# Optimization experiments

Hardware: AMD Instinct MI355X
Metric: run time of the kernel (lower is better)

Reference implementation:

```python
import jax, jax.numpy as jnp
import numpy as np

MODES = 256
WIDTH = 64
T_HIST = 1
T_FUT = 1
BATCH = 64
S = 8192


def setup_inputs() -> dict:
    key = jax.random.key(0)
    ks = jax.random.split(key, 12)
    scale = 1.0 / (WIDTH * WIDTH)
    inp = {
        "u": jax.random.normal(ks[0], (BATCH, S, T_HIST), dtype=jnp.float32),
        # lifting layer: Linear(T_HIST+1 -> WIDTH), stored [in, out]
        "fc0_w": jax.random.normal(ks[1], (T_HIST + 1, WIDTH), dtype=jnp.float32) * 0.5,
        "fc0_b": jax.random.normal(ks[2], (WIDTH,), dtype=jnp.float32) * 0.1,
        # 4 spectral conv layers, complex weights stored as real/imag parts
        "sw_r": scale * jax.random.uniform(ks[3], (4, WIDTH, WIDTH, MODES), dtype=jnp.float32),
        "sw_i": scale * jax.random.uniform(ks[4], (4, WIDTH, WIDTH, MODES), dtype=jnp.float32),
        # 4 pointwise (1x1 conv) layers: weight [out,in], bias [out]
        "pw_w": jax.random.normal(ks[5], (4, WIDTH, WIDTH), dtype=jnp.float32) * (1.0 / np.sqrt(WIDTH)),
        "pw_b": jax.random.normal(ks[6], (4, WIDTH), dtype=jnp.float32) * 0.1,
        # projection head
        "fc1_w": jax.random.normal(ks[7], (WIDTH, 128), dtype=jnp.float32) * (1.0 / np.sqrt(WIDTH)),
        "fc1_b": jax.random.normal(ks[8], (128,), dtype=jnp.float32) * 0.1,
        "fc2_w": jax.random.normal(ks[9], (128, T_FUT), dtype=jnp.float32) * (1.0 / np.sqrt(128)),
        "fc2_b": jax.random.normal(ks[10], (T_FUT,), dtype=jnp.float32) * 0.1,
    }
    return inp


def _spectral_conv(x, wr, wi):
    # x: [b, c_in, s] real; weights: [c_in, c_out, MODES] (real/imag parts)
    s = x.shape[-1]
    xf = jnp.fft.rfft(x)                     # [b, c_in, s//2+1] complex
    w = wr + 1j * wi
    om = jnp.einsum('bix,iox->box', xf[:, :, :MODES], w)  # [b, c_out, MODES]
    out_ft = jnp.zeros((x.shape[0], wr.shape[1], s // 2 + 1), dtype=om.dtype)
    out_ft = out_ft.at[:, :, :MODES].set(om)
    return jnp.fft.irfft(out_ft, n=s)        # [b, c_out, s] real


def reference(u, fc0_w, fc0_b, sw_r, sw_i, pw_w, pw_b, fc1_w, fc1_b, fc2_w, fc2_b):
    b, s, _ = u.shape
    grid = jnp.broadcast_to(jnp.linspace(0.0, 1.0, s, dtype=u.dtype)[None, :, None], (b, s, 1))
    x = jnp.concatenate([u, grid], axis=-1)              # [b, s, 2]
    x = x @ fc0_w + fc0_b                                # [b, s, W]
    x = jnp.transpose(x, (0, 2, 1))                      # [b, W, s]
    for l in range(4):
        x1 = _spectral_conv(x, sw_r[l], sw_i[l])
        x2 = jnp.einsum('oi,bis->bos', pw_w[l], x) + pw_b[l][None, :, None]
        x = x1 + x2
        if l < 3:
            x = jax.nn.gelu(x, approximate=False)
    x = jnp.transpose(x, (0, 2, 1))                      # [b, s, W]
    x = jax.nn.gelu(x @ fc1_w + fc1_b, approximate=False)
    x = x @ fc2_w + fc2_b                                # [b, s, T_FUT]
    return x
```

## Files before the change

### kernel.cpp

```cpp
#include <hip/hip_runtime.h>
#include <hip/hip_bf16.h>
#include <math.h>

#define BB 64
#define CC 64
#define SS 8192
#define HS 4096
#define NMODE 256
#define KK2 512

typedef __attribute__((ext_vector_type(8))) short short8;
typedef __attribute__((ext_vector_type(16))) float f32x16;

#define VMW8 asm volatile("s_waitcnt vmcnt(8)" ::: "memory")
#define VMW0 asm volatile("s_waitcnt vmcnt(0)" ::: "memory")
#define SBAR asm volatile("s_barrier" ::: "memory")

__device__ __forceinline__ float gelu_exact(float v) {
    return 0.5f * v * (1.0f + erff(v * 0.7071067811865476f));
}
__device__ __forceinline__ float b2f(ushort u) {
    return __uint_as_float(((unsigned int)u) << 16);
}
__device__ __forceinline__ ushort f2b(float v) {
    __hip_bfloat16 h = __float2bfloat16(v);
    return *(ushort*)&h;
}
__device__ __forceinline__ void split2(float v, ushort& h, ushort& l) {
    h = f2b(v);
    l = f2b(v - b2f(h));
}
__device__ __forceinline__ int colk(int c) {
    return (c < 256) ? (c & ~1) : (((c - 256) & ~1) | 1);
}
__device__ __forceinline__ void dma16(const ushort* g, ushort* l) {
    __builtin_amdgcn_global_load_lds((const __attribute__((address_space(1))) void*)g,
                                     (__attribute__((address_space(3))) void*)l, 16, 0, 0);
}

__global__ void build_T1p(ushort* __restrict__ h, ushort* __restrict__ l) {
    int c = blockIdx.x;
    int n = blockIdx.y * 256 + threadIdx.x;
    int k = colk(c), ri = c & 1;
    int m = (n * k) & (SS - 1);
    float th = (float)m * (6.283185307179586476925f / (float)SS);
    float s, co;
    sincosf(th, &s, &co);
    float v = ri ? -s : co;
    ushort hh, ll;
    split2(v, hh, ll);
    h[(size_t)c * HS + n] = hh;
    l[(size_t)c * HS + n] = ll;
}

__global__ void build_T2r(ushort* __restrict__ h, ushort* __restrict__ l) {
    int n = blockIdx.x;
    int c = blockIdx.y * 256 + threadIdx.x;
    int k = colk(c), ri = c & 1;
    int m = (n * k) & (SS - 1);
    float th = (float)m * (6.283185307179586476925f / (float)SS);
    float s, co;
    sincosf(th, &s, &co);
    float v = ri ? -s : co;
    ushort hh, ll;
    split2(v, hh, ll);
    h[(size_t)n * KK2 + c] = hh;
    l[(size_t)n * KK2 + c] = ll;
}

__global__ void zero_xf(float* __restrict__ p) {
    size_t i = ((size_t)blockIdx.x * 256 + threadIdx.x) * 4;
    *(float4*)&p[i] = make_float4(0.f, 0.f, 0.f, 0.f);
}

__global__ void lift_kernel(const float* __restrict__ u, const float* __restrict__ w0,
                            const float* __restrict__ b0, ushort* __restrict__ Eh,
                            ushort* __restrict__ El, ushort* __restrict__ Oh,
                            ushort* __restrict__ Ol) {
    int n = blockIdx.x * 256 + threadIdx.x;
    int c = blockIdx.y;
    int b = blockIdx.z;
    float g1 = (float)n * (1.0f / (float)(SS - 1));
    float g2 = (float)(n + HS) * (1.0f / (float)(SS - 1));
    float v1 = u[b * SS + n] * w0[c] + g1 * w0[CC + c] + b0[c];
    float v2 = u[b * SS + n + HS] * w0[c] + g2 * w0[CC + c] + b0[c];
    float E = v1 + v2, O = v1 - v2;
    ushort hh, ll;
    size_t idx = (size_t)(b * CC + c) * HS + n;
    split2(E, hh, ll);
    Eh[idx] = hh;
    El[idx] = ll;
    split2(O, hh, ll);
    Oh[idx] = hh;
    Ol[idx] = ll;
}

__global__ __launch_bounds__(256, 3) void dft_mfma(
    const ushort* __restrict__ Eh, const ushort* __restrict__ El,
    const ushort* __restrict__ Oh, const ushort* __restrict__ Ol,
    const ushort* __restrict__ t1h, const ushort* __restrict__ t1l,
    float* __restrict__ Xf) {
    __shared__ __align__(16) ushort SM[16384];
    ushort* As_h = SM;
    ushort* As_l = SM + 4096;
    ushort* Bs_h = SM + 8192;
    ushort* Bs_l = SM + 12288;
    const int t = threadIdx.x;
    const int L = blockIdx.x;
    const int gq = L >> 5, j = L & 31;
    const int c0 = (j >> 3) * 128;
    const int m0 = ((gq & 3) * 8 + (j & 7)) * 128;
    const int kz = (gq >> 2) * 1024;
    const ushort* __restrict__ Ahp = (c0 < 256) ? Eh : Oh;
    const ushort* __restrict__ Alp = (c0 < 256) ? El : Ol;
    const int lane = t & 63, w = t >> 6;
    const int wm = (w >> 1) * 64, wn = (w & 1) * 64;
    const int l32 = lane & 31, lh = lane >> 5;
    const int sr = t >> 1, sh = (t & 1) * 16;
    const int g0 = (t & 1) * 2;
    const int d0 = ((g0 + 0) * 128 + sr) * 8;
    const int d1 = ((g0 + 1) * 128 + sr) * 8;

    f32x16 acc[2][2];
#pragma unroll
    for (int i = 0; i < 2; i++)
#pragma unroll
        for (int jj = 0; jj < 2; jj++) acc[i][jj] = (f32x16)0.f;

    const size_t arow = (size_t)(m0 + sr) * HS;
    const size_t brow = (size_t)(c0 + sr) * HS;
    const int kend = kz + 1024;

    short8 a0h, a1h, a0l, a1l, b0h, b1h, b0l, b1l;
    {
        const size_t ga = arow + kz + sh;
        const size_t gb = brow + kz + sh;
        a0h = *(const short8*)&Ahp[ga];
        a1h = *(const short8*)&Ahp[ga + 8];
        a0l = *(const short8*)&Alp[ga];
        a1l = *(const short8*)&Alp[ga + 8];
        b0h = *(const short8*)&t1h[gb];
        b1h = *(const short8*)&t1h[gb + 8];
        b0l = *(const short8*)&t1l[gb];
        b1l = *(const short8*)&t1l[gb + 8];
    }
    for (int kt = kz; kt < kend; kt += 32) {
        __syncthreads();
        *(short8*)&As_h[d0] = a0h;
        *(short8*)&As_h[d1] = a1h;
        *(short8*)&As_l[d0] = a0l;
        *(short8*)&As_l[d1] = a1l;
        *(short8*)&Bs_h[d0] = b0h;
        *(short8*)&Bs_h[d1] = b1h;
        *(short8*)&Bs_l[d0] = b0l;
        *(short8*)&Bs_l[d1] = b1l;
        __syncthreads();
        const int ktn = (kt + 32 < kend) ? kt + 32 : kz;
        const size_t ga = arow + ktn + sh;
        const size_t gb = brow + ktn + sh;
        a0h = *(const short8*)&Ahp[ga];
        a1h = *(const short8*)&Ahp[ga + 8];
        a0l = *(const short8*)&Alp[ga];
        a1l = *(const short8*)&Alp[ga + 8];
        b0h = *(const short8*)&t1h[gb];
        b1h = *(const short8*)&t1h[gb + 8];
        b0l = *(const short8*)&t1l[gb];
        b1l = *(const short8*)&t1l[gb + 8];
#pragma unroll
        for (int s2 = 0; s2 < 2; s2++) {
            const int kg = s2 * 2 + lh;
            short8 ah[2], al[2], bh2[2], bl2[2];
#pragma unroll
            for (int mt = 0; mt < 2; mt++) {
                int off = (kg * 128 + wm + mt * 32 + l32) * 8;
                ah[mt] = *(const short8*)&As_h[off];
                al[mt] = *(const short8*)&As_l[off];
            }
#pragma unroll
            for (int nt = 0; nt < 2; nt++) {
                int off = (kg * 128 + wn + nt * 32 + l32) * 8;
                bh2[nt] = *(const short8*)&Bs_h[off];
                bl2[nt] = *(const short8*)&Bs_l[off];
            }
#pragma unroll
            for (int nt = 0; nt < 2; nt++)
#pragma unroll
                for (int mt = 0; mt < 2; mt++) {
                    acc[mt][nt] = __builtin_amdgcn_mfma_f32_32x32x16_bf16(ah[mt], bh2[nt], acc[mt][nt], 0, 0, 0);
                    acc[mt][nt] = __builtin_amdgcn_mfma_f32_32x32x16_bf16(ah[mt], bl2[nt], acc[mt][nt], 0, 0, 0);
                    acc[mt][nt] = __builtin_amdgcn_mfma_f32_32x32x16_bf16(al[mt], bh2[nt], acc[mt][nt], 0, 0, 0);
                }
        }
    }
#pragma unroll
    for (int mt = 0; mt < 2; mt++)
#pragma unroll
        for (int nt = 0; nt < 2; nt++) {
            int col = c0 + wn + nt * 32 + l32;
#pragma unroll
            for (int reg = 0; reg < 16; reg++) {
                int row = m0 + wm + mt * 32 + (reg & 3) + 8 * (reg >> 2) + 4 * lh;
                atomicAdd(&Xf[(size_t)row * KK2 + col], acc[mt][nt][reg]);
            }
        }
}

__global__ __launch_bounds__(256) void mode_mix(const float* __restrict__ Xf,
                                                const float* __restrict__ swr,
                                                const float* __restrict__ swi,
                                                ushort* __restrict__ omh,
                                                ushort* __restrict__ oml, int l) {
    int k = threadIdx.x;
    int bg = blockIdx.x * 2;
    int og = blockIdx.y * 2;
    const int cp = ((k & 1) << 8) | ((k >> 1) << 1);
    float ar[2][2] = {}, ai[2][2] = {};
#pragma unroll 2
    for (int i = 0; i < CC; i++) {
        float2 x0 = *(const float2*)&Xf[((size_t)(bg + 0) * CC + i) * KK2 + cp];
        float2 x1 = *(const float2*)&Xf[((size_t)(bg + 1) * CC + i) * KK2 + cp];
        size_t wb = ((size_t)(l * CC + i) * CC + og) * NMODE + k;
        float wr0 = swr[wb], wi0 = swi[wb];
        float wr1 = swr[wb + NMODE], wi1 = swi[wb + NMODE];
        ar[0][0] += x0.x * wr0 - x0.y * wi0;
        ai[0][0] += x0.x * wi0 + x0.y * wr0;
        ar[0][1] += x0.x * wr1 - x0.y * wi1;
        ai[0][1] += x0.x * wi1 + x0.y * wr1;
        ar[1][0] += x1.x * wr0 - x1.y * wi0;
        ai[1][0] += x1.x * wi0 + x1.y * wr0;
        ar[1][1] += x1.x * wr1 - x1.y * wi1;
        ai[1][1] += x1.x * wi1 + x1.y * wr1;
    }
    float ck = (k == 0) ? (1.0f / (float)SS) : (2.0f / (float)SS);
#pragma unroll
    for (int b2 = 0; b2 < 2; b2++)
#pragma unroll
        for (int oo = 0; oo < 2; oo++) {
            float re = ar[b2][oo] * ck;
            float im = ai[b2][oo] * ck;
            ushort hr, lr2, hi2, li2;
            split2(re, hr, lr2);
            split2(im, hi2, li2);
            size_t base = ((size_t)(bg + b2) * CC + og + oo) * KK2 + cp;
            *(ushort2*)&omh[base] = make_ushort2(hr, hi2);
            *(ushort2*)&oml[base] = make_ushort2(lr2, li2);
        }
}

__global__ __launch_bounds__(256, 2) void inv_mfma(
    const ushort* __restrict__ omh, const ushort* __restrict__ oml,
    const ushort* __restrict__ t2h, const ushort* __restrict__ t2l,
    const float* __restrict__ pww, const float* __restrict__ pwb,
    ushort* __restrict__ Eh, ushort* __restrict__ El,
    ushort* __restrict__ Oh, ushort* __restrict__ Ol, int l, int gel) {
    __shared__ __align__(16) ushort SM[32768];
    const int t = threadIdx.x;
    const int n0 = blockIdx.x * 128;
    const int row0 = blockIdx.y * 128;
    const int lane = t & 63, w = t >> 6;
    const int wm = (w >> 1) * 64, wn = (w & 1) * 64;
    const int l32 = lane & 31, lh = lane >> 5;

    f32x16 aP[2][2], aQ[2][2];
#pragma unroll
    for (int i = 0; i < 2; i++)
#pragma unroll
        for (int jj = 0; jj < 2; jj++) {
            aP[i][jj] = (f32x16)0.f;
            aQ[i][jj] = (f32x16)0.f;
        }

    const size_t aoff = (size_t)(row0 + lane) * KK2 + w * 8;
    const size_t boff = (size_t)(n0 + lane) * KK2 + w * 8;
    const size_t rstep = (size_t)64 * KK2;

    auto stage1 = [&](int st, int bsel) {
        const int kt = st * 32;
        ushort* base = SM + bsel * 16384;
        ushort* dAh = base + w * 1024;
        ushort* dAl = base + 4096 + w * 1024;
        ushort* dBh = base + 8192 + w * 1024;
        ushort* dBl = base + 12288 + w * 1024;
        dma16(omh + aoff + kt, dAh);
        dma16(omh + aoff + rstep + kt, dAh + 512);
        dma16(oml + aoff + kt, dAl);
        dma16(oml + aoff + rstep + kt, dAl + 512);
        dma16(t2h + boff + kt, dBh);
        dma16(t2h + boff + rstep + kt, dBh + 512);
        dma16(t2l + boff + kt, dBl);
        dma16(t2l + boff + rstep + kt, dBl + 512);
    };
    const size_t xsrc = (size_t)(row0 + (w >> 1) * 64 + (w & 1) * 32 + (lane >> 4)) * HS +
                        n0 + (lane & 15) * 8;
    auto stage2 = [&](const ushort* src, int bsel) {
        ushort* dX = SM + bsel * 16384 + w * 4096;
#pragma unroll
        for (int q = 0; q < 8; q++) dma16(src + xsrc + (size_t)q * 4 * HS, dX + q * 512);
    };
    auto compute1 = [&](f32x16 (&acc)[2][2], const int bsel) {
        const ushort* base = SM + bsel * 16384;
#pragma unroll
        for (int s2 = 0; s2 < 2; s2++) {
            const int kg = s2 * 2 + lh;
            short8 ah[2], al[2], bh2[2], bl2[2];
#pragma unroll
            for (int mt = 0; mt < 2; mt++) {
                int off = (kg * 128 + wm + mt * 32 + l32) * 8;
                ah[mt] = *(const short8*)&base[off];
                al[mt] = *(const short8*)&base[4096 + off];
            }
#pragma unroll
            for (int nt = 0; nt < 2; nt++) {
                int off = (kg * 128 + wn + nt * 32 + l32) * 8;
                bh2[nt] = *(const short8*)&base[8192 + off];
                bl2[nt] = *(const short8*)&base[12288 + off];
            }
#pragma unroll
            for (int nt = 0; nt < 2; nt++)
#pragma unroll
                for (int mt = 0; mt < 2; mt++) {
                    acc[mt][nt] = __builtin_amdgcn_mfma_f32_32x32x16_bf16(ah[mt], bh2[nt], acc[mt][nt], 0, 0, 0);
                    acc[mt][nt] = __builtin_amdgcn_mfma_f32_32x32x16_bf16(ah[mt], bl2[nt], acc[mt][nt], 0, 0, 0);
                    acc[mt][nt] = __builtin_amdgcn_mfma_f32_32x32x16_bf16(al[mt], bh2[nt], acc[mt][nt], 0, 0, 0);
                }
        }
    };

    stage1(0, 0);
#pragma unroll 1
    for (int st = 0; st < 8; st++) {
        const int buf = st & 1;
        stage1(st + 1, buf ^ 1);
        VMW8;
        SBAR;
        compute1(aP, buf);
        SBAR;
    }
#pragma unroll 1
    for (int st = 8; st < 15; st++) {
        const int buf = st & 1;
        stage1(st + 1, buf ^ 1);
        VMW8;
        SBAR;
        compute1(aQ, buf);
        SBAR;
    }
    {
        stage2(Eh, 0);
        VMW8;
        SBAR;
        compute1(aQ, 1);
        SBAR;
    }
#pragma unroll
    for (int mt = 0; mt < 2; mt++)
#pragma unroll
        for (int nt = 0; nt < 2; nt++) {
            f32x16 p = aP[mt][nt];
            aP[mt][nt] = p + aQ[mt][nt];
            aQ[mt][nt] = p - aQ[mt][nt];
        }
    short8 pah[4][2], pal[4][2];
#pragma unroll
    for (int ks = 0; ks < 4; ks++)
#pragma unroll
        for (int mt = 0; mt < 2; mt++) {
            const float* pp = &pww[(size_t)(l * CC + mt * 32 + l32) * CC + ks * 16 + lh * 8];
            float4 pa = *(const float4*)pp;
            float4 pb = *(const float4*)(pp + 4);
            float pv[8] = {pa.x, pa.y, pa.z, pa.w, pb.x, pb.y, pb.z, pb.w};
#pragma unroll
            for (int e = 0; e < 8; e++) {
                ushort h2, l2;
                split2(0.5f * pv[e], h2, l2);
                pah[ks][mt][e] = (short)h2;
                pal[ks][mt][e] = (short)l2;
            }
        }
    const int bsw = w >> 1;
    const ushort* const srcs[4] = {Eh, El, Oh, Ol};
#pragma unroll
    for (int r = 0; r < 4; r++) {
        const int buf = r & 1;
        const bool isO = (r >= 2), isHi = !(r & 1);
        if (r < 3) {
            stage2(srcs[r + 1], buf ^ 1);
            VMW8;
        } else {
            VMW0;
        }
        SBAR;
        const ushort* base = SM + buf * 16384;
#pragma unroll
        for (int ks = 0; ks < 4; ks++) {
            short8 bf[2], nbf[2];
#pragma unroll
            for (int nt = 0; nt < 2; nt++) {
                const int rb = (bsw * 64 + ks * 16 + lh * 8) * 128 + wn + nt * 32 + l32;
#pragma unroll
                for (int jj = 0; jj < 8; jj++) bf[nt][jj] = (short)base[rb + jj * 128];
                if (isO) {
#pragma unroll
                    for (int jj = 0; jj < 8; jj++)
                        nbf[nt][jj] = (short)(bf[nt][jj] ^ (short)0x8000);
                }
            }
#pragma unroll
            for (int nt = 0; nt < 2; nt++)
#pragma unroll
                for (int mt = 0; mt < 2; mt++) {
                    aP[mt][nt] = __builtin_amdgcn_mfma_f32_32x32x16_bf16(pah[ks][mt], bf[nt], aP[mt][nt], 0, 0, 0);
                    aQ[mt][nt] = __builtin_amdgcn_mfma_f32_32x32x16_bf16(pah[ks][mt], isO ? nbf[nt] : bf[nt], aQ[mt][nt], 0, 0, 0);
                    if (isHi) {
                        aP[mt][nt] = __builtin_amdgcn_mfma_f32_32x32x16_bf16(pal[ks][mt], bf[nt], aP[mt][nt], 0, 0, 0);
                        aQ[mt][nt] = __builtin_amdgcn_mfma_f32_32x32x16_bf16(pal[ks][mt], isO ? nbf[nt] : bf[nt], aQ[mt][nt], 0, 0, 0);
                    }
                }
        }
        if (r < 3) SBAR;
    }
#pragma unroll
    for (int mt = 0; mt < 2; mt++)
#pragma unroll
        for (int nt = 0; nt < 2; nt++)
#pragma unroll
            for (int reg = 0; reg < 16; reg++) {
                int roffs = (reg & 3) + 8 * (reg >> 2) + 4 * lh;
                float bias = pwb[l * CC + mt * 32 + roffs];
                float uu = aP[mt][nt][reg] + bias;
                float vv = aQ[mt][nt][reg] + bias;
                if (gel) {
                    uu = gelu_exact(uu);
                    vv = gelu_exact(vv);
                }
                float EE = uu + vv, OO = uu - vv;
                ushort h2, l2;
                size_t gg = (size_t)(row0 + wm + mt * 32 + roffs) * HS + n0 + wn + nt * 32 + l32;
                split2(EE, h2, l2);
                Eh[gg] = h2;
                El[gg] = l2;
                split2(OO, h2, l2);
                Oh[gg] = h2;
                Ol[gg] = l2;
            }
}

__global__ __launch_bounds__(256, 3) void head_kernel(
    const ushort* __restrict__ Eh, const ushort* __restrict__ El,
    const ushort* __restrict__ Oh, const ushort* __restrict__ Ol,
    const float* __restrict__ w1, const float* __restrict__ b1,
    const float* __restrict__ w2, const float* __restrict__ b2,
    float* __restrict__ out) {
    __shared__ __align__(16) ushort Xh[4096];
    __shared__ __align__(16) ushort Xl[4096];
    __shared__ __align__(16) ushort Wh[8192];
    __shared__ __align__(16) ushort Wl[8192];
    __shared__ float part[4][64];
    const int b = blockIdx.y;
    const int n0 = blockIdx.x * 64;
    const int t = threadIdx.x;
    const int lane = t & 63, w = t >> 6;
    const int l32 = lane & 31, lh = lane >> 5;
    const float sg = (n0 < HS) ? 0.5f : -0.5f;
    const int nc = n0 & (HS - 1);
    {
        const int n = lane;
        const size_t gx = (size_t)(b * CC + w * 16) * HS + nc + n;
        short8 fh[2], fl[2];
#pragma unroll
        for (int cc = 0; cc < 16; cc++) {
            size_t g = gx + (size_t)cc * HS;
            float e = b2f(Eh[g]) + b2f(El[g]);
            float o = b2f(Oh[g]) + b2f(Ol[g]);
            float x = 0.5f * e + sg * o;
            ushort hh, ll;
            split2(x, hh, ll);
            fh[cc >> 3][cc & 7] = (short)hh;
            fl[cc >> 3][cc & 7] = (short)ll;
        }
        const int kg0 = w * 2;
#pragma unroll
        for (int q = 0; q < 2; q++) {
            *(short8*)&Xh[((kg0 + q) * 64 + n) * 8] = fh[q];
            *(short8*)&Xl[((kg0 + q) * 64 + n) * 8] = fl[q];
        }
    }
    {
        const int j = t & 127, half = t >> 7;
#pragma unroll
        for (int q = 0; q < 4; q++) {
            const int kg = half * 4 + q;
            short8 fh, fl;
#pragma unroll
            for (int e = 0; e < 8; e++) {
                int c = kg * 8 + e;
                ushort hh, ll;
                split2(w1[c * 128 + j], hh, ll);
                fh[e] = (short)hh;
                fl[e] = (short)ll;
            }
            *(short8*)&Wh[(kg * 128 + j) * 8] = fh;
            *(short8*)&Wl[(kg * 128 + j) * 8] = fl;
        }
    }
    __syncthreads();
    f32x16 acc[2];
    acc[0] = (f32x16)0.f;
    acc[1] = (f32x16)0.f;
#pragma unroll
    for (int ks = 0; ks < 4; ks++) {
        const int kg = ks * 2 + lh;
        const int offa = (kg * 128 + w * 32 + l32) * 8;
        short8 awh = *(const short8*)&Wh[offa];
        short8 awl = *(const short8*)&Wl[offa];
#pragma unroll
        for (int nt = 0; nt < 2; nt++) {
            const int offb = (kg * 64 + nt * 32 + l32) * 8;
            short8 bxh = *(const short8*)&Xh[offb];
            short8 bxl = *(const short8*)&Xl[offb];
            acc[nt] = __builtin_amdgcn_mfma_f32_32x32x16_bf16(awh, bxh, acc[nt], 0, 0, 0);
            acc[nt] = __builtin_amdgcn_mfma_f32_32x32x16_bf16(awh, bxl, acc[nt], 0, 0, 0);
            acc[nt] = __builtin_amdgcn_mfma_f32_32x32x16_bf16(awl, bxh, acc[nt], 0, 0, 0);
        }
    }
#pragma unroll
    for (int nt = 0; nt < 2; nt++) {
        float s = 0.f;
#pragma unroll
        for (int reg = 0; reg < 16; reg++) {
            const int j0 = w * 32 + (reg & 3) + 8 * (reg >> 2) + 4 * lh;
            s += gelu_exact(acc[nt][reg] + b1[j0]) * w2[j0];
        }
        s += __shfl_xor(s, 32);
        part[w][nt * 32 + l32] = s;
    }
    __syncthreads();
    if (t < 64)
        out[b * SS + n0 + t] = part[0][t] + part[1][t] + part[2][t] + part[3][t] + b2[0];
}

extern "C" void kernel_launch(void* const* d_in, const int* in_sizes, int n_in,
                              void* d_out, int out_size, void* d_ws, size_t ws_size,
                              hipStream_t stream) {
    (void)in_sizes; (void)n_in; (void)out_size; (void)ws_size;
    const float* u = (const float*)d_in[0];
    const float* fc0_w = (const float*)d_in[1];
    const float* fc0_b = (const float*)d_in[2];
    const float* sw_r = (const float*)d_in[3];
    const float* sw_i = (const float*)d_in[4];
    const float* pw_w = (const float*)d_in[5];
    const float* pw_b = (const float*)d_in[6];
    const float* fc1_w = (const float*)d_in[7];
    const float* fc1_b = (const float*)d_in[8];
    const float* fc2_w = (const float*)d_in[9];
    const float* fc2_b = (const float*)d_in[10];
    float* out = (float*)d_out;

    char* ws = (char*)d_ws;
    ushort* Eh = (ushort*)ws;
    ushort* El = (ushort*)(ws + 33554432);
    ushort* Oh = (ushort*)(ws + 67108864);
    ushort* Ol = (ushort*)(ws + 100663296);
    ushort* t1h = (ushort*)(ws + 134217728);
    ushort* t1l = (ushort*)(ws + 138412032);
    ushort* t2h = (ushort*)(ws + 142606336);
    ushort* t2l = (ushort*)(ws + 146800640);
    ushort* omh = (ushort*)(ws + 150994944);
    ushort* oml = (ushort*)(ws + 155189248);
    float* Xf = (float*)(ws + 159383552);

    build_T1p<<<dim3(KK2, HS / 256), 256, 0, stream>>>(t1h, t1l);
    build_T2r<<<dim3(HS, KK2 / 256), 256, 0, stream>>>(t2h, t2l);
    lift_kernel<<<dim3(HS / 256, CC, BB), 256, 0, stream>>>(u, fc0_w, fc0_b, Eh, El,
                                                            Oh, Ol);
    for (int l = 0; l < 4; l++) {
        zero_xf<<<dim3(2048), 256, 0, stream>>>(Xf);
        dft_mfma<<<dim3(512), 256, 0, stream>>>(Eh, El, Oh, Ol, t1h, t1l, Xf);
        mode_mix<<<dim3(BB / 2, CC / 2), 256, 0, stream>>>(Xf, sw_r, sw_i, omh, oml, l);
        inv_mfma<<<dim3(HS / 128, 32), 256, 0, stream>>>(
            omh, oml, t2h, t2l, pw_w, pw_b, Eh, El, Oh, Ol, l, (l < 3) ? 1 : 0);
    }
    head_kernel<<<dim3(SS / 64, BB), 256, 0, stream>>>(Eh, El, Oh, Ol, fc1_w, fc1_b,
                                                       fc2_w, fc2_b, out);
}
```

Measured before the change: 1.281 ms.

## Split inv_mfma across two warp groups with one accumulator set each, exchanged via LDS

inv_mfma goes from 256 to 512 threads. Two 4-wave groups each keep a single accumulator set: one handles the even half of the K range, the other the odd half. They combine into the sum and difference through LDS before the pointwise stage and again before the epilogue writes. This halves accumulator registers per wave so more waves can be resident (launch bounds 512,4). The low-part weight split is now recomputed inside the loop to save registers. The cost is extra LDS round trips and barriers, and the r-loop is no longer unrolled.

```diff
diff --git a/kernel.cpp b/kernel.cpp
--- a/kernel.cpp
+++ b/kernel.cpp
@@ -12,7 +12,7 @@
 typedef __attribute__((ext_vector_type(8))) short short8;
 typedef __attribute__((ext_vector_type(16))) float f32x16;
 
-#define VMW8 asm volatile("s_waitcnt vmcnt(8)" ::: "memory")
+#define VMW4 asm volatile("s_waitcnt vmcnt(4)" ::: "memory")
 #define VMW0 asm volatile("s_waitcnt vmcnt(0)" ::: "memory")
 #define SBAR asm volatile("s_barrier" ::: "memory")
 
@@ -247,7 +247,7 @@
         }
 }
 
-__global__ __launch_bounds__(256, 2) void inv_mfma(
+__global__ __launch_bounds__(512, 4) void inv_mfma(
     const ushort* __restrict__ omh, const ushort* __restrict__ oml,
     const ushort* __restrict__ t2h, const ushort* __restrict__ t2l,
     const float* __restrict__ pww, const float* __restrict__ pwb,
@@ -258,109 +258,115 @@
     const int n0 = blockIdx.x * 128;
     const int row0 = blockIdx.y * 128;
     const int lane = t & 63, w = t >> 6;
-    const int wm = (w >> 1) * 64, wn = (w & 1) * 64;
+    const int grp = w >> 2, w2 = w & 3;
+    const int wm = (w2 >> 1) * 64, wn = (w2 & 1) * 64;
     const int l32 = lane & 31, lh = lane >> 5;
 
-    f32x16 aP[2][2], aQ[2][2];
+    f32x16 acc[2][2];
 #pragma unroll
     for (int i = 0; i < 2; i++)
 #pragma unroll
-        for (int jj = 0; jj < 2; jj++) {
-            aP[i][jj] = (f32x16)0.f;
-            aQ[i][jj] = (f32x16)0.f;
-        }
-
-    const size_t aoff = (size_t)(row0 + lane) * KK2 + w * 8;
-    const size_t boff = (size_t)(n0 + lane) * KK2 + w * 8;
-    const size_t rstep = (size_t)64 * KK2;
+        for (int jj = 0; jj < 2; jj++) acc[i][jj] = (f32x16)0.f;
+
+    const ushort* const arrs1[4] = {omh, oml, t2h, t2l};
+    const ushort* const sa = arrs1[w2];
+    const int rowbase = (w2 < 2) ? row0 : n0;
+    const size_t s1off = (size_t)(rowbase + lane) * KK2 + grp * 256;
+    const size_t r64 = (size_t)64 * KK2;
 
     auto stage1 = [&](int st, int bsel) {
-        const int kt = st * 32;
-        ushort* base = SM + bsel * 16384;
-        ushort* dAh = base + w * 1024;
-        ushort* dAl = base + 4096 + w * 1024;
-        ushort* dBh = base + 8192 + w * 1024;
-        ushort* dBl = base + 12288 + w * 1024;
-        dma16(omh + aoff + kt, dAh);
-        dma16(omh + aoff + rstep + kt, dAh + 512);
-        dma16(oml + aoff + kt, dAl);
-        dma16(oml + aoff + rstep + kt, dAl + 512);
-        dma16(t2h + boff + kt, dBh);
-        dma16(t2h + boff + rstep + kt, dBh + 512);
-        dma16(t2l + boff + kt, dBl);
-        dma16(t2l + boff + rstep + kt, dBl + 512);
+        const int kt = st * 16;
+        ushort* dst = SM + bsel * 16384 + grp * 8192 + w2 * 2048;
+        const size_t s0 = s1off + kt;
+        dma16(sa + s0, dst);
+        dma16(sa + s0 + r64, dst + 512);
+        dma16(sa + s0 + 8, dst + 1024);
+        dma16(sa + s0 + r64 + 8, dst + 1536);
     };
-    const size_t xsrc = (size_t)(row0 + (w >> 1) * 64 + (w & 1) * 32 + (lane >> 4)) * HS +
-                        n0 + (lane & 15) * 8;
+    const size_t x2off = (size_t)(row0 + grp * 64 + w2 * 16 + (lane >> 4)) * HS +
+                         n0 + (lane & 15) * 8;
     auto stage2 = [&](const ushort* src, int bsel) {
-        ushort* dX = SM + bsel * 16384 + w * 4096;
-#pragma unroll
-        for (int q = 0; q < 8; q++) dma16(src + xsrc + (size_t)q * 4 * HS, dX + q * 512);
+        ushort* dst = SM + bsel * 16384 + w * 2048;
+#pragma unroll
+        for (int q = 0; q < 4; q++) dma16(src + x2off + (size_t)q * 4 * HS, dst + q * 512);
     };
-    auto compute1 = [&](f32x16 (&acc)[2][2], const int bsel) {
-        const ushort* base = SM + bsel * 16384;
-#pragma unroll
-        for (int s2 = 0; s2 < 2; s2++) {
-            const int kg = s2 * 2 + lh;
-            short8 ah[2], al[2], bh2[2], bl2[2];
+    auto compute1 = [&](int bsel) {
+        const ushort* bA_h = SM + bsel * 16384 + grp * 8192;
+        const ushort* bA_l = bA_h + 2048;
+        const ushort* bB_h = bA_h + 4096;
+        const ushort* bB_l = bA_h + 6144;
+        short8 ah[2], al[2], bh2[2], bl2[2];
+#pragma unroll
+        for (int mt = 0; mt < 2; mt++) {
+            const int off = (lh * 128 + wm + mt * 32 + l32) * 8;
+            ah[mt] = *(const short8*)&bA_h[off];
+            al[mt] = *(const short8*)&bA_l[off];
+        }
+#pragma unroll
+        for (int nt = 0; nt < 2; nt++) {
+            const int off = (lh * 128 + wn + nt * 32 + l32) * 8;
+            bh2[nt] = *(const short8*)&bB_h[off];
+            bl2[nt] = *(const short8*)&bB_l[off];
+        }
+#pragma unroll
+        for (int nt = 0; nt < 2; nt++)
 #pragma unroll
             for (int mt = 0; mt < 2; mt++) {
-                int off = (kg * 128 + wm + mt * 32 + l32) * 8;
-                ah[mt] = *(const short8*)&base[off];
-                al[mt] = *(const short8*)&base[4096 + off];
-            }
-#pragma unroll
-            for (int nt = 0; nt < 2; nt++) {
-                int off = (kg * 128 + wn + nt * 32 + l32) * 8;
-                bh2[nt] = *(const short8*)&base[8192 + off];
-                bl2[nt] = *(const short8*)&base[12288 + off];
-            }
-#pragma unroll
-            for (int nt = 0; nt < 2; nt++)
-#pragma unroll
-                for (int mt = 0; mt < 2; mt++) {
-                    acc[mt][nt] = __builtin_amdgcn_mfma_f32_32x32x16_bf16(ah[mt], bh2[nt], acc[mt][nt], 0, 0, 0);
-                    acc[mt][nt] = __builtin_amdgcn_mfma_f32_32x32x16_bf16(ah[mt], bl2[nt], acc[mt][nt], 0, 0, 0);
-                    acc[mt][nt] = __builtin_amdgcn_mfma_f32_32x32x16_bf16(al[mt], bh2[nt], acc[mt][nt], 0, 0, 0);
-                }
-        }
+                acc[mt][nt] = __builtin_amdgcn_mfma_f32_32x32x16_bf16(ah[mt], bh2[nt], acc[mt][nt], 0, 0, 0);
+                acc[mt][nt] = __builtin_amdgcn_mfma_f32_32x32x16_bf16(ah[mt], bl2[nt], acc[mt][nt], 0, 0, 0);
+                acc[mt][nt] = __builtin_amdgcn_mfma_f32_32x32x16_bf16(al[mt], bh2[nt], acc[mt][nt], 0, 0, 0);
+            }
     };
 
     stage1(0, 0);
 #pragma unroll 1
-    for (int st = 0; st < 8; st++) {
+    for (int st = 0; st < 15; st++) {
         const int buf = st & 1;
         stage1(st + 1, buf ^ 1);
-        VMW8;
+        VMW4;
         SBAR;
-        compute1(aP, buf);
-        SBAR;
-    }
-#pragma unroll 1
-    for (int st = 8; st < 15; st++) {
-        const int buf = st & 1;
-        stage1(st + 1, buf ^ 1);
-        VMW8;
-        SBAR;
-        compute1(aQ, buf);
+        compute1(buf);
         SBAR;
     }
     {
         stage2(Eh, 0);
-        VMW8;
+        VMW4;
         SBAR;
-        compute1(aQ, 1);
+        compute1(1);
         SBAR;
     }
-#pragma unroll
-    for (int mt = 0; mt < 2; mt++)
-#pragma unroll
-        for (int nt = 0; nt < 2; nt++) {
-            f32x16 p = aP[mt][nt];
-            aP[mt][nt] = p + aQ[mt][nt];
-            aQ[mt][nt] = p - aQ[mt][nt];
-        }
-    short8 pah[4][2], pal[4][2];
+    {
+        float4* XB = (float4*)(SM + 16384);
+        const int slot = grp * 4 + w2, pslot = (grp ^ 1) * 4 + w2;
+#pragma unroll
+        for (int mt = 0; mt < 2; mt++)
+#pragma unroll
+            for (int nt = 0; nt < 2; nt++) {
+#pragma unroll
+                for (int r = 0; r < 4; r++)
+                    XB[(r * 8 + slot) * 64 + lane] =
+                        make_float4(acc[mt][nt][4 * r + 0], acc[mt][nt][4 * r + 1],
+                                    acc[mt][nt][4 * r + 2], acc[mt][nt][4 * r + 3]);
+                SBAR;
+#pragma unroll
+                for (int r = 0; r < 4; r++) {
+                    float4 o = XB[(r * 8 + pslot) * 64 + lane];
+                    if (grp == 0) {
+                        acc[mt][nt][4 * r + 0] += o.x;
+                        acc[mt][nt][4 * r + 1] += o.y;
+                        acc[mt][nt][4 * r + 2] += o.z;
+                        acc[mt][nt][4 * r + 3] += o.w;
+                    } else {
+                        acc[mt][nt][4 * r + 0] = o.x - acc[mt][nt][4 * r + 0];
+                        acc[mt][nt][4 * r + 1] = o.y - acc[mt][nt][4 * r + 1];
+                        acc[mt][nt][4 * r + 2] = o.z - acc[mt][nt][4 * r + 2];
+                        acc[mt][nt][4 * r + 3] = o.w - acc[mt][nt][4 * r + 3];
+                    }
+                }
+                SBAR;
+            }
+    }
+    short8 pah[4][2];
 #pragma unroll
     for (int ks = 0; ks < 4; ks++)
 #pragma unroll
@@ -370,22 +376,17 @@
             float4 pb = *(const float4*)(pp + 4);
             float pv[8] = {pa.x, pa.y, pa.z, pa.w, pb.x, pb.y, pb.z, pb.w};
 #pragma unroll
-            for (int e = 0; e < 8; e++) {
-                ushort h2, l2;
-                split2(0.5f * pv[e], h2, l2);
-                pah[ks][mt][e] = (short)h2;
-                pal[ks][mt][e] = (short)l2;
-            }
-        }
-    const int bsw = w >> 1;
+            for (int e = 0; e < 8; e++) pah[ks][mt][e] = (short)f2b(0.5f * pv[e]);
+        }
+    const int bsw = w2 >> 1;
     const ushort* const srcs[4] = {Eh, El, Oh, Ol};
-#pragma unroll
+#pragma unroll 1
     for (int r = 0; r < 4; r++) {
         const int buf = r & 1;
         const bool isO = (r >= 2), isHi = !(r & 1);
         if (r < 3) {
             stage2(srcs[r + 1], buf ^ 1);
-            VMW8;
+            VMW4;
         } else {
             VMW0;
         }
@@ -393,56 +394,84 @@
         const ushort* base = SM + buf * 16384;
 #pragma unroll
         for (int ks = 0; ks < 4; ks++) {
-            short8 bf[2], nbf[2];
+            short8 bf[2];
 #pragma unroll
             for (int nt = 0; nt < 2; nt++) {
                 const int rb = (bsw * 64 + ks * 16 + lh * 8) * 128 + wn + nt * 32 + l32;
 #pragma unroll
                 for (int jj = 0; jj < 8; jj++) bf[nt][jj] = (short)base[rb + jj * 128];
-                if (isO) {
-#pragma unroll
-                    for (int jj = 0; jj < 8; jj++)
-                        nbf[nt][jj] = (short)(bf[nt][jj] ^ (short)0x8000);
+                if (isO && grp == 1) {
+#pragma unroll
+                    for (int jj = 0; jj < 8; jj++) bf[nt][jj] = (short)(bf[nt][jj] ^ (short)0x8000);
                 }
             }
 #pragma unroll
             for (int nt = 0; nt < 2; nt++)
 #pragma unroll
+                for (int mt = 0; mt < 2; mt++)
+                    acc[mt][nt] = __builtin_amdgcn_mfma_f32_32x32x16_bf16(pah[ks][mt], bf[nt], acc[mt][nt], 0, 0, 0);
+            if (isHi) {
+#pragma unroll
                 for (int mt = 0; mt < 2; mt++) {
-                    aP[mt][nt] = __builtin_amdgcn_mfma_f32_32x32x16_bf16(pah[ks][mt], bf[nt], aP[mt][nt], 0, 0, 0);
-                    aQ[mt][nt] = __builtin_amdgcn_mfma_f32_32x32x16_bf16(pah[ks][mt], isO ? nbf[nt] : bf[nt], aQ[mt][nt], 0, 0, 0);
-                    if (isHi) {
-                        aP[mt][nt] = __builtin_amdgcn_mfma_f32_32x32x16_bf16(pal[ks][mt], bf[nt], aP[mt][nt], 0, 0, 0);
-                        aQ[mt][nt] = __builtin_amdgcn_mfma_f32_32x32x16_bf16(pal[ks][mt], isO ? nbf[nt] : bf[nt], aQ[mt][nt], 0, 0, 0);
+                    const float* pp = &pww[(size_t)(l * CC + mt * 32 + l32) * CC + ks * 16 + lh * 8];
+                    float4 pa = *(const float4*)pp;
+                    float4 pb = *(const float4*)(pp + 4);
+                    float pv[8] = {pa.x, pa.y, pa.z, pa.w, pb.x, pb.y, pb.z, pb.w};
+                    short8 palm;
+#pragma unroll
+                    for (int e = 0; e < 8; e++) {
+                        float v = 0.5f * pv[e];
+                        palm[e] = (short)f2b(v - b2f((ushort)pah[ks][mt][e]));
+                    }
+#pragma unroll
+                    for (int nt = 0; nt < 2; nt++)
+                        acc[mt][nt] = __builtin_amdgcn_mfma_f32_32x32x16_bf16(palm, bf[nt], acc[mt][nt], 0, 0, 0);
+                }
+            }
+        }
+        if (r < 3) SBAR;
+    }
+    {
+        float4* EB = (float4*)SM;
+        const int slot = grp * 4 + w2, pslot = (grp ^ 1) * 4 + w2;
+        ushort* const dstH = grp ? Oh : Eh;
+        ushort* const dstL = grp ? Ol : El;
+#pragma unroll
+        for (int mt = 0; mt < 2; mt++)
+#pragma unroll
+            for (int nt = 0; nt < 2; nt++) {
+                float tmp[16];
+#pragma unroll
+                for (int reg = 0; reg < 16; reg++) {
+                    const int roffs = (reg & 3) + 8 * (reg >> 2) + 4 * lh;
+                    float tv = acc[mt][nt][reg] + pwb[l * CC + mt * 32 + roffs];
+                    tmp[reg] = gel ? gelu_exact(tv) : tv;
+                }
+#pragma unroll
+                for (int r = 0; r < 4; r++)
+                    EB[(r * 8 + slot) * 64 + lane] =
+                        make_float4(tmp[4 * r + 0], tmp[4 * r + 1], tmp[4 * r + 2], tmp[4 * r + 3]);
+                SBAR;
+#pragma unroll
+                for (int r = 0; r < 4; r++) {
+                    float4 o = EB[(r * 8 + pslot) * 64 + lane];
+                    float ov[4] = {o.x, o.y, o.z, o.w};
+#pragma unroll
+                    for (int j = 0; j < 4; j++) {
+                        const int reg = 4 * r + j;
+                        const int roffs = (reg & 3) + 8 * (reg >> 2) + 4 * lh;
+                        float res = (grp == 0) ? (tmp[reg] + ov[j]) : (ov[j] - tmp[reg]);
+                        ushort h2, l2;
+                        split2(res, h2, l2);
+                        const size_t gg = (size_t)(row0 + wm + mt * 32 + roffs) * HS +
+                                          n0 + wn + nt * 32 + l32;
+                        dstH[gg] = h2;
+                        dstL[gg] = l2;
                     }
                 }
-        }
-        if (r < 3) SBAR;
-    }
-#pragma unroll
-    for (int mt = 0; mt < 2; mt++)
-#pragma unroll
-        for (int nt = 0; nt < 2; nt++)
-#pragma unroll
-            for (int reg = 0; reg < 16; reg++) {
-                int roffs = (reg & 3) + 8 * (reg >> 2) + 4 * lh;
-                float bias = pwb[l * CC + mt * 32 + roffs];
-                float uu = aP[mt][nt][reg] + bias;
-                float vv = aQ[mt][nt][reg] + bias;
-                if (gel) {
-                    uu = gelu_exact(uu);
-                    vv = gelu_exact(vv);
-                }
-                float EE = uu + vv, OO = uu - vv;
-                ushort h2, l2;
-                size_t gg = (size_t)(row0 + wm + mt * 32 + roffs) * HS + n0 + wn + nt * 32 + l32;
-                split2(EE, h2, l2);
-                Eh[gg] = h2;
-                El[gg] = l2;
-                split2(OO, h2, l2);
-                Oh[gg] = h2;
-                Ol[gg] = l2;
-            }
+                if (!(mt == 1 && nt == 1)) SBAR;
+            }
+    }
 }
 
 __global__ __launch_bounds__(256, 3) void head_kernel(
@@ -577,7 +606,7 @@
         zero_xf<<<dim3(2048), 256, 0, stream>>>(Xf);
         dft_mfma<<<dim3(512), 256, 0, stream>>>(Eh, El, Oh, Ol, t1h, t1l, Xf);
         mode_mix<<<dim3(BB / 2, CC / 2), 256, 0, stream>>>(Xf, sw_r, sw_i, omh, oml, l);
-        inv_mfma<<<dim3(HS / 128, 32), 256, 0, stream>>>(
+        inv_mfma<<<dim3(HS / 128, 32), 512, 0, stream>>>(
             omh, oml, t2h, t2l, pw_w, pw_b, Eh, El, Oh, Ol, l, (l < 3) ? 1 : 0);
     }
     head_kernel<<<dim3(SS / 64, BB), 256, 0, stream>>>(Eh, El, Oh, Ol, fc1_w, fc1_b,
```

Result: slower. 1.907 ms (+48.9%).

## Double-buffer DFT GEMM tiles with direct global-to-LDS loads

Applied to the files above, without the earlier changes.

Replaces the register-staged global→LDS copy in the DFT MFMA kernel with direct global-to-LDS DMA (dma16) into two LDS buffers. The next k-tile is prefetched while the current one is computed, using vmcnt waits and raw barriers instead of two __syncthreads per step. LDS use doubles to 64KB per block, so the occupancy hint drops from 3 to 2 blocks per CU. This trades latency hiding for occupancy.

```diff
diff --git a/kernel.cpp b/kernel.cpp
--- a/kernel.cpp
+++ b/kernel.cpp
@@ -95,16 +95,12 @@
     Ol[idx] = ll;
 }
 
-__global__ __launch_bounds__(256, 3) void dft_mfma(
+__global__ __launch_bounds__(256, 2) void dft_mfma(
     const ushort* __restrict__ Eh, const ushort* __restrict__ El,
     const ushort* __restrict__ Oh, const ushort* __restrict__ Ol,
     const ushort* __restrict__ t1h, const ushort* __restrict__ t1l,
     float* __restrict__ Xf) {
-    __shared__ __align__(16) ushort SM[16384];
-    ushort* As_h = SM;
-    ushort* As_l = SM + 4096;
-    ushort* Bs_h = SM + 8192;
-    ushort* Bs_l = SM + 12288;
+    __shared__ __align__(16) ushort SM[32768];
     const int t = threadIdx.x;
     const int L = blockIdx.x;
     const int gq = L >> 5, j = L & 31;
@@ -116,10 +112,6 @@
     const int lane = t & 63, w = t >> 6;
     const int wm = (w >> 1) * 64, wn = (w & 1) * 64;
     const int l32 = lane & 31, lh = lane >> 5;
-    const int sr = t >> 1, sh = (t & 1) * 16;
-    const int g0 = (t & 1) * 2;
-    const int d0 = ((g0 + 0) * 128 + sr) * 8;
-    const int d1 = ((g0 + 1) * 128 + sr) * 8;
 
     f32x16 acc[2][2];
 #pragma unroll
@@ -127,45 +119,30 @@
 #pragma unroll
         for (int jj = 0; jj < 2; jj++) acc[i][jj] = (f32x16)0.f;
 
-    const size_t arow = (size_t)(m0 + sr) * HS;
-    const size_t brow = (size_t)(c0 + sr) * HS;
-    const int kend = kz + 1024;
-
-    short8 a0h, a1h, a0l, a1l, b0h, b1h, b0l, b1l;
-    {
-        const size_t ga = arow + kz + sh;
-        const size_t gb = brow + kz + sh;
-        a0h = *(const short8*)&Ahp[ga];
-        a1h = *(const short8*)&Ahp[ga + 8];
-        a0l = *(const short8*)&Alp[ga];
-        a1l = *(const short8*)&Alp[ga + 8];
-        b0h = *(const short8*)&t1h[gb];
-        b1h = *(const short8*)&t1h[gb + 8];
-        b0l = *(const short8*)&t1l[gb];
-        b1l = *(const short8*)&t1l[gb + 8];
-    }
-    for (int kt = kz; kt < kend; kt += 32) {
-        __syncthreads();
-        *(short8*)&As_h[d0] = a0h;
-        *(short8*)&As_h[d1] = a1h;
-        *(short8*)&As_l[d0] = a0l;
-        *(short8*)&As_l[d1] = a1l;
-        *(short8*)&Bs_h[d0] = b0h;
-        *(short8*)&Bs_h[d1] = b1h;
-        *(short8*)&Bs_l[d0] = b0l;
-        *(short8*)&Bs_l[d1] = b1l;
-        __syncthreads();
-        const int ktn = (kt + 32 < kend) ? kt + 32 : kz;
-        const size_t ga = arow + ktn + sh;
-        const size_t gb = brow + ktn + sh;
-        a0h = *(const short8*)&Ahp[ga];
-        a1h = *(const short8*)&Ahp[ga + 8];
-        a0l = *(const short8*)&Alp[ga];
-        a1l = *(const short8*)&Alp[ga + 8];
-        b0h = *(const short8*)&t1h[gb];
-        b1h = *(const short8*)&t1h[gb + 8];
-        b0l = *(const short8*)&t1l[gb];
-        b1l = *(const short8*)&t1l[gb + 8];
+    const size_t aoff = (size_t)(m0 + lane) * HS + w * 8;
+    const size_t boff = (size_t)(c0 + lane) * HS + w * 8;
+    const size_t r64 = (size_t)64 * HS;
+
+    auto stage = [&](int kt, int bsel) {
+        ushort* base = SM + bsel * 16384;
+        ushort* dAh = base + w * 1024;
+        ushort* dAl = base + 4096 + w * 1024;
+        ushort* dBh = base + 8192 + w * 1024;
+        ushort* dBl = base + 12288 + w * 1024;
+        dma16(Ahp + aoff + kt, dAh);
+        dma16(Ahp + aoff + r64 + kt, dAh + 512);
+        dma16(Alp + aoff + kt, dAl);
+        dma16(Alp + aoff + r64 + kt, dAl + 512);
+        dma16(t1h + boff + kt, dBh);
+        dma16(t1h + boff + r64 + kt, dBh + 512);
+        dma16(t1l + boff + kt, dBl);
+        dma16(t1l + boff + r64 + kt, dBl + 512);
+    };
+    auto compute = [&](int bsel) {
+        const ushort* As_h = SM + bsel * 16384;
+        const ushort* As_l = As_h + 4096;
+        const ushort* Bs_h = As_h + 8192;
+        const ushort* Bs_l = As_h + 12288;
 #pragma unroll
         for (int s2 = 0; s2 < 2; s2++) {
             const int kg = s2 * 2 + lh;
@@ -191,6 +168,21 @@
                     acc[mt][nt] = __builtin_amdgcn_mfma_f32_32x32x16_bf16(al[mt], bh2[nt], acc[mt][nt], 0, 0, 0);
                 }
         }
+    };
+
+    stage(kz, 0);
+#pragma unroll 1
+    for (int st = 0; st < 32; st++) {
+        const int buf = st & 1;
+        if (st < 31) {
+            stage(kz + (st + 1) * 32, buf ^ 1);
+            VMW8;
+        } else {
+            VMW0;
+        }
+        SBAR;
+        compute(buf);
+        SBAR;
     }
 #pragma unroll
     for (int mt = 0; mt < 2; mt++)
```

Result: slower. 1.315 ms (+2.6%).
